# Performance work log

Measured on AMD Instinct MI355X. Metric: run time of the kernel, lower is better.

## Reference

```python
import jax, jax.numpy as jnp
import numpy as np

TEMPERATURE_F = 0.5


def setup_inputs() -> dict:
    key = jax.random.key(0)
    k1, k2, k3, k4, k5 = jax.random.split(key, 5)
    B, D, K = 4096, 128, 8192
    return {
        "h_i": jax.random.normal(k1, (B, D), dtype=jnp.float32),
        "h_j": jax.random.normal(k2, (B, D), dtype=jnp.float32),
        "sub_graph": jax.random.uniform(k3, (B, K), dtype=jnp.float32),
        "sub_x": jax.random.normal(k4, (B, D), dtype=jnp.float32),
        "all_x": jax.random.normal(k5, (K, D), dtype=jnp.float32),
    }


def _forward_feature(h_i, h_j):
    # NT-Xent contrastive loss (CrossEntropyLoss with label 0, reduction='sum', /N).
    B = h_i.shape[0]
    N = 2 * B
    h = jnp.concatenate([h_i, h_j], axis=0)           # [N, D]
    sim = (h @ h.T) / TEMPERATURE_F                   # [N, N]
    idx = jnp.arange(N)
    pos = sim[idx, (idx + B) % N]                     # positives: diag(sim, +B) ++ diag(sim, -B)
    # logits row i = [pos_i] ++ {sim[i,j] : j != i, j != i±B}. Since pos_i == sim[i, i±B],
    # the logsumexp over that row equals logsumexp over sim[i,:] with only the diagonal removed.
    sim_nodiag = jnp.where(jnp.eye(N, dtype=bool), -jnp.inf, sim)
    lse = jax.nn.logsumexp(sim_nodiag, axis=1)        # [N]
    return jnp.sum(lse - pos) / N


def _graph_loss(sub_graph, sub_x, all_x):
    # trace(X^T diag(r) X) = sum_i r_i * ||X_i||^2 ; trace(A^T G B) = sum(G * (A B^T)) = sum((G B) * A)
    r = jnp.sum(sub_graph, axis=1)                    # [M]
    c = jnp.sum(sub_graph, axis=0)                    # [K]
    t1 = jnp.sum(r * jnp.sum(sub_x * sub_x, axis=1))
    t2 = jnp.sum(c * jnp.sum(all_x * all_x, axis=1))
    t3 = jnp.sum((sub_graph @ all_x) * sub_x)         # trace(sub_x^T G all_x)
    M, K = sub_graph.shape
    return (t1 + t2 - 2.0 * t3) / (M * K)


def reference(h_i, h_j, sub_graph, sub_x, all_x):
    contrastive = _forward_feature(h_i, h_j)
    graph = _graph_loss(sub_graph, sub_x, all_x)
    return contrastive + graph
```

## Files before the change

kernel.cpp:

```cpp
#include <hip/hip_runtime.h>
#include <hip/hip_bf16.h>

typedef __attribute__((ext_vector_type(4)))  float f32x4;
typedef __attribute__((ext_vector_type(16))) float f32x16;
typedef __attribute__((ext_vector_type(8)))  short s16x8;
typedef unsigned short u16;
typedef unsigned int u32;

#define ALPHA 1.6986436f
#define LN2F  0.69314718056f
#define COFF  128.0f

__device__ __forceinline__ u16 f2bf(float x) {
  union { float f; u32 u; } v; v.f = x;
  u32 r = v.u + 0x7fffu + ((v.u >> 16) & 1u);
  return (u16)(r >> 16);
}

#if __has_builtin(__builtin_amdgcn_exp2f)
__device__ __forceinline__ float fexp2(float x) { return __builtin_amdgcn_exp2f(x); }
#else
__device__ __forceinline__ float fexp2(float x) { return exp2f(x); }
#endif
#if __has_builtin(__builtin_amdgcn_logf)
__device__ __forceinline__ float flog2(float x) { return __builtin_amdgcn_logf(x); }
#else
__device__ __forceinline__ float flog2(float x) { return log2f(x); }
#endif

__device__ __forceinline__ s16x8 cvt8(float4 a, float4 b) {
  union { u32 w[4]; s16x8 v; } u;
  asm("v_cvt_pk_bf16_f32 %0, %1, %2" : "=v"(u.w[0]) : "v"(a.x), "v"(a.y));
  asm("v_cvt_pk_bf16_f32 %0, %1, %2" : "=v"(u.w[1]) : "v"(a.z), "v"(a.w));
  asm("v_cvt_pk_bf16_f32 %0, %1, %2" : "=v"(u.w[2]) : "v"(b.x), "v"(b.y));
  asm("v_cvt_pk_bf16_f32 %0, %1, %2" : "=v"(u.w[3]) : "v"(b.z), "v"(b.w));
  return u.v;
}

__device__ __forceinline__ f32x16 mfma32(s16x8 a, s16x8 b, f32x16 c) {
  return __builtin_amdgcn_mfma_f32_32x32x16_bf16(a, b, c, 0, 0, 0);
}
__device__ __forceinline__ f32x16 zero16() {
  f32x16 z;
#pragma unroll
  for (int i = 0; i < 16; ++i) z[i] = 0.f;
  return z;
}
__device__ __forceinline__ void gl16(const void* g, void* l) {
  __builtin_amdgcn_global_load_lds(
      (const __attribute__((address_space(1))) u32*)g,
      (__attribute__((address_space(3))) u32*)l, 16, 0, 0);
}

__global__ __launch_bounds__(256)
void prep_all(const float* __restrict__ h_i, const float* __restrict__ h_j,
              const float* __restrict__ all_x, const float* __restrict__ subx,
              u16* __restrict__ hbf, u16* __restrict__ axKT, u16* __restrict__ sxb,
              float* __restrict__ nall, float* __restrict__ nsub,
              float* __restrict__ pos4) {
  int bid = blockIdx.x, tid = threadIdx.x;
  if (bid < 512) {
    int t = bid * 256 + tid;
    int row = t >> 4, kb = t & 15;
    const float* src = (row < 4096 ? h_i + (size_t)row * 128
                                   : h_j + (size_t)(row - 4096) * 128) + kb * 8;
    float4 f0 = *(const float4*)(src);
    float4 f1 = *(const float4*)(src + 4);
    float4 sa = {ALPHA * f0.x, ALPHA * f0.y, ALPHA * f0.z, ALPHA * f0.w};
    float4 sb = {ALPHA * f1.x, ALPHA * f1.y, ALPHA * f1.z, ALPHA * f1.w};
    s16x8 o = cvt8(sa, sb);
    char* dst = (char*)hbf + (size_t)row * 256 + ((kb * 16) ^ ((row & 7) << 4));
    *(s16x8*)dst = o;
    if (row < 4096) {
      const float* srcj = h_j + (size_t)row * 128 + kb * 8;
      float4 g0 = *(const float4*)(srcj);
      float4 g1 = *(const float4*)(srcj + 4);
      float dp = f0.x * g0.x + f0.y * g0.y + f0.z * g0.z + f0.w * g0.w
               + f1.x * g1.x + f1.y * g1.y + f1.z * g1.z + f1.w * g1.w;
      dp += __shfl_xor(dp, 1, 64);
      dp += __shfl_xor(dp, 2, 64);
      dp += __shfl_xor(dp, 4, 64);
      dp += __shfl_xor(dp, 8, 64);
      if ((tid & 15) == 0) pos4[row] = 2.0f * dp;
    }
  } else if (bid < 640) {
    int ab = bid - 512;
    {
      int kk = ab * 64 + (tid >> 2), q = tid & 3;
      const float* p = all_x + (size_t)kk * 128 + q * 32;
      float s = 0.f;
#pragma unroll
      for (int c = 0; c < 8; ++c) {
        float4 v = ((const float4*)p)[c];
        s += v.x * v.x + v.y * v.y + v.z * v.z + v.w * v.w;
      }
      s += __shfl_xor(s, 1, 64);
      s += __shfl_xor(s, 2, 64);
      if (q == 0) nall[kk] = s;
    }
#pragma unroll
    for (int j = 0; j < 2; ++j) {
      int c = ab * 512 + tid * 2 + j;
      int k = c >> 3, dc = c & 7;
      const float* p = all_x + (size_t)k * 128 + dc * 16;
      float4 a0 = ((const float4*)p)[0];
      float4 a1 = ((const float4*)p)[1];
      float4 a2 = ((const float4*)p)[2];
      float4 a3 = ((const float4*)p)[3];
      *(s16x8*)((char*)axKT + (size_t)dc * 262144 + (size_t)k * 32)      = cvt8(a0, a1);
      *(s16x8*)((char*)axKT + (size_t)dc * 262144 + (size_t)k * 32 + 16) = cvt8(a2, a3);
    }
  } else {
    int t = (bid - 640) * 256 + tid;
    int row = t >> 4, kb = t & 15;
    const float* src = subx + (size_t)row * 128 + kb * 8;
    float4 f0 = *(const float4*)(src);
    float4 f1 = *(const float4*)(src + 4);
    *(s16x8*)((char*)sxb + (size_t)row * 256 + kb * 16) = cvt8(f0, f1);
    float dp = f0.x * f0.x + f0.y * f0.y + f0.z * f0.z + f0.w * f0.w
             + f1.x * f1.x + f1.y * f1.y + f1.z * f1.z + f1.w * f1.w;
    dp += __shfl_xor(dp, 1, 64);
    dp += __shfl_xor(dp, 2, 64);
    dp += __shfl_xor(dp, 4, 64);
    dp += __shfl_xor(dp, 8, 64);
    if ((tid & 15) == 0) nsub[row] = dp;
  }
}

__global__ __launch_bounds__(256)
void contrast_k(const u16* __restrict__ hbf, float* __restrict__ spart) {
  __shared__ char clds[2][8192];
  int bid = blockIdx.x, tid = threadIdx.x;
  int lane = tid & 63, w = tid >> 6, il = lane & 31, hi = lane >> 5;
  int rt = bid >> 5, oct = bid & 31;
  int C0 = oct * 256;
  int rowbase = rt * 256 + w * 64;
  s16x8 bf0[8], bf1[8];
#pragma unroll
  for (int rs = 0; rs < 2; ++rs) {
    int r = rowbase + rs * 32 + il;
    const char* rp = (const char*)hbf + (size_t)r * 256;
    int sw = (r & 7) << 4;
#pragma unroll
    for (int ks = 0; ks < 8; ++ks) {
      s16x8 v = *(const s16x8*)(rp + ((ks * 32 + hi * 16) ^ sw));
      if (rs == 0) bf0[ks] = v; else bf1[ks] = v;
    }
  }
  float s0 = 0.f, s1 = 0.f;
  auto stage = [&](int buf, int t) {
    const char* src = (const char*)hbf + (size_t)(C0 + t * 32) * 256 + tid * 16;
    char* dst = &clds[buf][0] + tid * 16;
    gl16(src, dst);
    gl16(src + 4096, dst + 4096);
  };
  stage(0, 0);
  __syncthreads();
  int cur = 0;
  for (int t = 0; t < 8; ++t) {
    if (t < 7) stage(cur ^ 1, t + 1);
    const char* basep = &clds[cur][0];
    s16x8 af[8];
#pragma unroll
    for (int ks = 0; ks < 8; ++ks)
      af[ks] = *(const s16x8*)(basep + il * 256 + ((ks * 32 + hi * 16) ^ ((il & 7) << 4)));
    f32x16 A0 = zero16(), A1 = zero16();
#pragma unroll
    for (int ks = 0; ks < 8; ++ks) {
      A0 = mfma32(af[ks], bf0[ks], A0);
      A1 = mfma32(af[ks], bf1[ks], A1);
    }
    int cb = C0 + t * 32;
    bool d0 = (cb == rowbase), d1 = (cb == rowbase + 32);
    if (!(d0 | d1)) {
#pragma unroll
      for (int r = 0; r < 16; ++r) {
        s0 += fexp2(A0[r] - COFF);
        s1 += fexp2(A1[r] - COFF);
      }
    } else {
#pragma unroll
      for (int r = 0; r < 16; ++r) {
        int jc = (r & 3) + 8 * (r >> 2) + 4 * hi;
        float t0 = fexp2(A0[r] - COFF);
        float t1 = fexp2(A1[r] - COFF);
        if (d0 && jc == il) t0 = 0.f;
        if (d1 && jc == il) t1 = 0.f;
        s0 += t0; s1 += t1;
      }
    }
    __syncthreads();
    cur ^= 1;
  }
  s0 += __shfl_xor(s0, 32, 64);
  s1 += __shfl_xor(s1, 32, 64);
  if (hi == 0) {
    spart[oct * 8192 + rowbase + il]      = s0;
    spart[oct * 8192 + rowbase + 32 + il] = s1;
  }
}

__global__ __launch_bounds__(256)
void graph_k(const float* __restrict__ G, const u16* __restrict__ sxb,
             const u16* __restrict__ axKT, const float* __restrict__ nall,
             const float* __restrict__ nsub, float* __restrict__ gpart) {
  __shared__ float wsum[4];
  int bid = blockIdx.x, tid = threadIdx.x;
  int lane = tid & 63, w = tid >> 6, il = lane & 31, hi = lane >> 5;
  int rb = bid >> 2, kq = bid & 3;
  int i0 = rb * 32;
  int k0w = kq * 2048 + w * 512;

  s16x8 A[8];
#pragma unroll
  for (int dc = 0; dc < 8; ++dc)
    A[dc] = *(const s16x8*)((const char*)sxb + (size_t)(i0 + il) * 256 + dc * 32 + hi * 16);

  float ns[16];
#pragma unroll
  for (int r = 0; r < 16; ++r)
    ns[r] = nsub[i0 + (r & 3) + 8 * (r >> 2) + 4 * hi];

  const char* aktB = (const char*)axKT + il * 32 + hi * 16;
  const float* gB = G + (size_t)i0 * 8192 + il;
  const float* nlB = nall + il;

  float s = 0.f;
  float g0[16], g1[16], g2[16];
  float nk0, nk1, nk2;
  s16x8 B0[8], B1[8];

#define GLOAD(T, GR, NK)                                                     \
  { int k_ = k0w + (T) * 32;                                                 \
    _Pragma("unroll")                                                        \
    for (int r = 0; r < 16; ++r)                                             \
      GR[r] = gB[(size_t)(((r & 3) + 8 * (r >> 2) + 4 * hi) * 8192 + k_)];   \
    NK = nlB[k_]; }

#define BLOAD(T, BR)                                                         \
  { int k_ = k0w + (T) * 32;                                                 \
    _Pragma("unroll")                                                        \
    for (int dc = 0; dc < 8; ++dc)                                           \
      BR[dc] = *(const s16x8*)(aktB + (size_t)dc * 262144 + (size_t)k_ * 32); }

#define GSTEP(T, GR, NK, BR)                                                 \
  { f32x16 E = zero16();                                                     \
    _Pragma("unroll")                                                        \
    for (int dc = 0; dc < 8; ++dc) E = mfma32(A[dc], BR[dc], E);             \
    _Pragma("unroll")                                                        \
    for (int r = 0; r < 16; ++r)                                             \
      s = fmaf(GR[r], fmaf(-2.f, E[r], ns[r] + NK), s);                      \
    if ((T) + 2 <= 15) BLOAD((T) + 2, BR);                                   \
    if ((T) + 3 <= 15) GLOAD((T) + 3, GR, NK); }

  GLOAD(0, g0, nk0);
  BLOAD(0, B0);
  GLOAD(1, g1, nk1);
  BLOAD(1, B1);
  GLOAD(2, g2, nk2);

  GSTEP(0,  g0, nk0, B0)
  GSTEP(1,  g1, nk1, B1)
  GSTEP(2,  g2, nk2, B0)
  GSTEP(3,  g0, nk0, B1)
  GSTEP(4,  g1, nk1, B0)
  GSTEP(5,  g2, nk2, B1)
  GSTEP(6,  g0, nk0, B0)
  GSTEP(7,  g1, nk1, B1)
  GSTEP(8,  g2, nk2, B0)
  GSTEP(9,  g0, nk0, B1)
  GSTEP(10, g1, nk1, B0)
  GSTEP(11, g2, nk2, B1)
  GSTEP(12, g0, nk0, B0)
  GSTEP(13, g1, nk1, B1)
  GSTEP(14, g2, nk2, B0)
  GSTEP(15, g0, nk0, B1)
#undef GSTEP
#undef BLOAD
#undef GLOAD

#pragma unroll
  for (int d = 1; d < 64; d <<= 1) s += __shfl_xor(s, d, 64);
  if (lane == 0) wsum[w] = s;
  __syncthreads();
  if (tid == 0) gpart[bid] = wsum[0] + wsum[1] + wsum[2] + wsum[3];
}

__global__ __launch_bounds__(256)
void epilogue1(const float* __restrict__ spart, const float* __restrict__ pos4,
               float* __restrict__ cpart) {
  int tid = threadIdx.x;
  int row = blockIdx.x * 256 + tid;
  float S = 0.f;
#pragma unroll
  for (int o = 0; o < 32; ++o) S += spart[o * 8192 + row];
  float c = LN2F * (COFF + flog2(S)) - pos4[row & 4095];
#pragma unroll
  for (int d = 1; d < 64; d <<= 1) c += __shfl_xor(c, d, 64);
  __shared__ float ws4[4];
  int l = tid & 63, w = tid >> 6;
  if (l == 0) ws4[w] = c;
  __syncthreads();
  if (tid == 0) cpart[blockIdx.x] = ws4[0] + ws4[1] + ws4[2] + ws4[3];
}

__global__ __launch_bounds__(256)
void final_sum(const float* __restrict__ cpart, const float* __restrict__ gpart,
               float* __restrict__ out) {
  int tid = threadIdx.x;
  double gd = 0.0;
  for (int idx = tid; idx < 512; idx += 256) gd += (double)gpart[idx];
  double cd = (tid < 32) ? (double)cpart[tid] : 0.0;
#pragma unroll
  for (int d = 1; d < 64; d <<= 1) {
    cd += __shfl_xor(cd, d, 64);
    gd += __shfl_xor(gd, d, 64);
  }
  __shared__ double wc[4], wg[4];
  int l = tid & 63, w = tid >> 6;
  if (l == 0) { wc[w] = cd; wg[w] = gd; }
  __syncthreads();
  if (tid == 0) {
    double C = wc[0] + wc[1] + wc[2] + wc[3];
    double Gs = wg[0] + wg[1] + wg[2] + wg[3];
    out[0] = (float)(C / 8192.0 + Gs / (4096.0 * 8192.0));
  }
}

extern "C" void kernel_launch(void* const* d_in, const int* in_sizes, int n_in,
                              void* d_out, int out_size, void* d_ws, size_t ws_size,
                              hipStream_t stream) {
  const float* h_i = (const float*)d_in[0];
  const float* h_j = (const float*)d_in[1];
  const float* G   = (const float*)d_in[2];
  const float* sx  = (const float*)d_in[3];
  const float* ax  = (const float*)d_in[4];
  char* ws = (char*)d_ws;
  u16*   hbf   = (u16*)(ws);
  u16*   axKT  = (u16*)(ws + 2097152);
  u16*   sxb   = (u16*)(ws + 4194304);
  float* nall  = (float*)(ws + 5242880);
  float* nsub  = (float*)(ws + 5275648);
  float* pos4  = (float*)(ws + 5292032);
  float* spart = (float*)(ws + 5308416);
  float* gpart = (float*)(ws + 6356992);
  float* cpart = (float*)(ws + 6359040);
  float* out = (float*)d_out;

  prep_all<<<dim3(896), dim3(256), 0, stream>>>(h_i, h_j, ax, sx, hbf, axKT, sxb,
                                                nall, nsub, pos4);
  contrast_k<<<dim3(1024), dim3(256), 0, stream>>>(hbf, spart);
  graph_k<<<dim3(512), dim3(256), 0, stream>>>(G, sxb, axKT, nall, nsub, gpart);
  epilogue1<<<dim3(32), dim3(256), 0, stream>>>(spart, pos4, cpart);
  final_sum<<<dim3(1), dim3(256), 0, stream>>>(cpart, gpart, out);
}
```

Before: 60.13 us.

## Exploit symmetry of similarity matrix to halve contrastive tile work

The contrastive kernel now computes only the upper-triangular block pairs of the symmetric sim matrix (528 blocks instead of 1024). Off-diagonal blocks contribute their exp values to both the row sums and the column sums, the latter reduced with cross-lane shuffles and shared memory and written to separate partial slots. This roughly halves the MFMA and exp work, at the cost of extra shuffle reductions, shared-memory traffic and a more complex partial-sum layout. The epilogue must read the added slots for the result to be correct.

```diff
diff --git a/kernel.cpp b/kernel.cpp
--- a/kernel.cpp
+++ b/kernel.cpp
@@ -130,11 +130,15 @@
 __global__ __launch_bounds__(256)
 void contrast_k(const u16* __restrict__ hbf, float* __restrict__ spart) {
   __shared__ char clds[2][8192];
+  __shared__ float colsumW[4][256];
   int bid = blockIdx.x, tid = threadIdx.x;
   int lane = tid & 63, w = tid >> 6, il = lane & 31, hi = lane >> 5;
-  int rt = bid >> 5, oct = bid & 31;
-  int C0 = oct * 256;
-  int rowbase = rt * 256 + w * 64;
+  int a, o;
+  if (bid < 512) { a = bid & 31; o = bid >> 5; }
+  else           { a = bid - 512; o = 16; }
+  int b = (a + o) & 31;
+  int C0 = b * 256;
+  int rowbase = a * 256 + w * 64;
   s16x8 bf0[8], bf1[8];
 #pragma unroll
   for (int rs = 0; rs < 2; ++rs) {
@@ -170,15 +174,9 @@
       A0 = mfma32(af[ks], bf0[ks], A0);
       A1 = mfma32(af[ks], bf1[ks], A1);
     }
-    int cb = C0 + t * 32;
-    bool d0 = (cb == rowbase), d1 = (cb == rowbase + 32);
-    if (!(d0 | d1)) {
-#pragma unroll
-      for (int r = 0; r < 16; ++r) {
-        s0 += fexp2(A0[r] - COFF);
-        s1 += fexp2(A1[r] - COFF);
-      }
-    } else {
+    if (o == 0) {
+      int cb = C0 + t * 32;
+      bool d0 = (cb == rowbase), d1 = (cb == rowbase + 32);
 #pragma unroll
       for (int r = 0; r < 16; ++r) {
         int jc = (r & 3) + 8 * (r >> 2) + 4 * hi;
@@ -188,6 +186,20 @@
         if (d1 && jc == il) t1 = 0.f;
         s0 += t0; s1 += t1;
       }
+    } else {
+#pragma unroll
+      for (int r = 0; r < 16; ++r) {
+        float e0 = fexp2(A0[r] - COFF);
+        float e1 = fexp2(A1[r] - COFF);
+        s0 += e0; s1 += e1;
+        float cv = e0 + e1;
+        cv += __shfl_xor(cv, 1, 64);
+        cv += __shfl_xor(cv, 2, 64);
+        cv += __shfl_xor(cv, 4, 64);
+        cv += __shfl_xor(cv, 8, 64);
+        cv += __shfl_xor(cv, 16, 64);
+        if (il == r) colsumW[w][t * 32 + ((r & 3) + 8 * (r >> 2) + 4 * hi)] = cv;
+      }
     }
     __syncthreads();
     cur ^= 1;
@@ -195,8 +207,13 @@
   s0 += __shfl_xor(s0, 32, 64);
   s1 += __shfl_xor(s1, 32, 64);
   if (hi == 0) {
-    spart[oct * 8192 + rowbase + il]      = s0;
-    spart[oct * 8192 + rowbase + 32 + il] = s1;
+    spart[o * 8192 + rowbase + il]      = s0;
+    spart[o * 8192 + rowbase + 32 + il] = s1;
+  }
+  if (o != 0) {
+    int slot2 = (o == 16) ? 16 : 16 + o;
+    float c = colsumW[0][tid] + colsumW[1][tid] + colsumW[2][tid] + colsumW[3][tid];
+    spart[slot2 * 8192 + C0 + tid] = c;
   }
 }
 
@@ -349,7 +366,7 @@
 
   prep_all<<<dim3(896), dim3(256), 0, stream>>>(h_i, h_j, ax, sx, hbf, axKT, sxb,
                                                 nall, nsub, pos4);
-  contrast_k<<<dim3(1024), dim3(256), 0, stream>>>(hbf, spart);
+  contrast_k<<<dim3(528), dim3(256), 0, stream>>>(hbf, spart);
   graph_k<<<dim3(512), dim3(256), 0, stream>>>(G, sxb, axKT, nall, nsub, gpart);
   epilogue1<<<dim3(32), dim3(256), 0, stream>>>(spart, pos4, cpart);
   final_sum<<<dim3(1), dim3(256), 0, stream>>>(cpart, gpart, out);
```

New measurement: 81.30 us. 35.2% more time.
